# Kernel tuning notes

Hardware: AMD Instinct MI355X
Metric: run time of the kernel (lower is better)

The kernel has to match this reference:

```python
import jax, jax.numpy as jnp
import numpy as np

D_MODEL = 256
D_STATE = 16
D_CONV = 3
D_INNER = 256          # expand=1
D_HALF = D_INNER // 2  # 128
DT_RANK = 16           # ceil(256/16)
B, L0, L1 = 4, 4096, 4096


def setup_inputs() -> dict:
    key = jax.random.key(0)
    ks = jax.random.split(key, 10)
    u_0 = jax.random.normal(ks[0], (B, L0, D_MODEL), jnp.float32)
    u_1 = jax.random.normal(ks[1], (B, L1, D_MODEL), jnp.float32)
    in_proj_w = jax.random.normal(ks[2], (D_INNER, D_MODEL), jnp.float32) * (D_MODEL ** -0.5)
    conv_x_w = jax.random.normal(ks[3], (D_HALF, 1, D_CONV), jnp.float32) * (D_CONV ** -0.5)
    conv_z_w = jax.random.normal(ks[4], (D_HALF, 1, D_CONV), jnp.float32) * (D_CONV ** -0.5)
    x_proj_w = jax.random.normal(ks[5], (DT_RANK + 2 * D_STATE, D_HALF), jnp.float32) * (D_HALF ** -0.5)
    dt_init_std = DT_RANK ** -0.5
    dt_proj_w = jax.random.uniform(ks[6], (D_HALF, DT_RANK), jnp.float32, -dt_init_std, dt_init_std)
    # dt bias = inverse-softplus of dt ~ LogUniform(1e-3, 1e-1)
    dt = jnp.exp(jax.random.uniform(ks[7], (D_HALF,), jnp.float32) * (np.log(0.1) - np.log(0.001)) + np.log(0.001))
    dt = jnp.clip(dt, 1e-4, None)
    dt_proj_b = dt + jnp.log(-jnp.expm1(-dt))
    A_log = jnp.log(jnp.broadcast_to(jnp.arange(1, D_STATE + 1, dtype=jnp.float32), (D_HALF, D_STATE)))
    D_param = jnp.ones((D_HALF,), jnp.float32)
    out_proj_w = jax.random.normal(ks[8], (D_MODEL, D_INNER), jnp.float32) * (D_INNER ** -0.5)
    return {"u_0": u_0, "u_1": u_1, "in_proj_w": in_proj_w, "conv_x_w": conv_x_w,
            "conv_z_w": conv_z_w, "x_proj_w": x_proj_w, "dt_proj_w": dt_proj_w,
            "dt_proj_b": dt_proj_b, "A_log": A_log, "D": D_param, "out_proj_w": out_proj_w}


def _dwconv(x, w):
    # x: [B, C, L], w: [C, 1, K] depthwise, padding='same', no bias (conv_bias//2 == 0)
    return jax.lax.conv_general_dilated(
        x, w, window_strides=(1,), padding='SAME',
        feature_group_count=x.shape[1], dimension_numbers=('NCH', 'OIH', 'NCH'))


def _selective_scan(u, delta, A, Bm, Cm, Dv):
    # u, delta: [B, L, d]; A: [d, n]; Bm, Cm: [B, L, n]; Dv: [d]
    dA = jnp.exp(delta[..., None] * A)                       # [B, L, d, n]
    dBu = (delta * u)[..., None] * Bm[:, :, None, :]         # [B, L, d, n]
    def combine(c1, c2):
        a1, b1 = c1
        a2, b2 = c2
        return a2 * a1, a2 * b1 + b2
    _, h = jax.lax.associative_scan(combine, (dA, dBu), axis=1)  # h: [B, L, d, n]
    return jnp.einsum('bldn,bln->bld', h, Cm) + u * Dv


def _stream(u, in_proj_w, conv_x_w, conv_z_w, x_proj_w, dt_proj_w, dt_proj_b, A, D, out_proj_w):
    xz = jnp.einsum('bld,ed->ble', u, in_proj_w)             # [B, L, d_inner]
    x, z = jnp.split(xz, 2, axis=-1)                         # [B, L, d_half] each
    x = jnp.swapaxes(x, 1, 2)                                # [B, d_half, L]
    z = jnp.swapaxes(z, 1, 2)
    x_f = jax.nn.silu(_dwconv(x, conv_x_w))
    z_f = jax.nn.silu(_dwconv(z, conv_z_w))
    xf = jnp.swapaxes(x_f, 1, 2)                             # [B, L, d_half]
    dbl = jnp.einsum('bld,ed->ble', xf, x_proj_w)            # [B, L, dt_rank + 2n]
    dt, Bm, Cm = jnp.split(dbl, [DT_RANK, DT_RANK + D_STATE], axis=-1)
    dt = jnp.einsum('blr,dr->bld', dt, dt_proj_w)
    delta = jax.nn.softplus(dt + dt_proj_b)                  # delta_bias + delta_softplus
    y = _selective_scan(xf, delta, A, Bm, Cm, D)             # [B, L, d_half]
    cat = jnp.concatenate([y, jnp.swapaxes(z_f, 1, 2)], axis=-1)  # [B, L, d_inner]
    return jnp.einsum('ble,oe->blo', cat, out_proj_w)


def reference(u_0, u_1, in_proj_w, conv_x_w, conv_z_w, x_proj_w, dt_proj_w, dt_proj_b, A_log, D, out_proj_w):
    A = -jnp.exp(A_log)
    out0 = _stream(u_0, in_proj_w, conv_x_w, conv_z_w, x_proj_w, dt_proj_w, dt_proj_b, A, D, out_proj_w)
    out1 = _stream(u_1, in_proj_w, conv_x_w, conv_z_w, x_proj_w, dt_proj_w, dt_proj_b, A, D, out_proj_w)
    return (out0, out1)
```

## Files before the change

### kernel.cpp

```cpp
#include <hip/hip_runtime.h>
#include <hip/hip_bf16.h>
#include <cstdint>

#define DEV __device__ __forceinline__

typedef __attribute__((ext_vector_type(8))) short short8;
typedef __attribute__((ext_vector_type(4))) float f32x4;
typedef __attribute__((ext_vector_type(4))) unsigned short us4;
typedef __attribute__((ext_vector_type(8))) unsigned short us8;

DEV unsigned short f2bf(float x) {
    unsigned int u = __float_as_uint(x);
    unsigned int r = (u + 0x7FFFu + ((u >> 16) & 1u)) >> 16;
    return (unsigned short)r;
}
DEV float bf2f(unsigned short h) { return __uint_as_float(((unsigned int)h) << 16); }

#define LL 4096
#define DM 256
#define DH 128
#define NS 16
#define SB_TOT 8
#define CH1 32
#define NCH 128
#define LOG2E 1.44269504088896f

__global__ __launch_bounds__(256) void prep_w(
    const float* __restrict__ xpw, const float* __restrict__ dtw,
    unsigned short* __restrict__ Wb)
{
    int gid = blockIdx.x * 256 + threadIdx.x;
    if (gid >= 5120) return;
    int n = gid >> 5, k0 = (gid & 31) * 4;
    if (n < 128) {
        float a0 = 0.f, a1 = 0.f, a2 = 0.f, a3 = 0.f;
        const float* dw = dtw + n * 16;
        #pragma unroll
        for (int r = 0; r < 16; ++r) {
            float w = dw[r];
            const float* xr = xpw + r * 128 + k0;
            a0 = fmaf(w, xr[0], a0);
            a1 = fmaf(w, xr[1], a1);
            a2 = fmaf(w, xr[2], a2);
            a3 = fmaf(w, xr[3], a3);
        }
        us4 rr = { f2bf(a0), f2bf(a1), f2bf(a2), f2bf(a3) };
        *(us4*)&Wb[n * 128 + k0] = rr;
    } else {
        f32x4 v = *(const f32x4*)&xpw[(n - 112) * 128 + k0];
        us4 rr = { f2bf(v.x), f2bf(v.y), f2bf(v.z), f2bf(v.w) };
        *(us4*)&Wb[n * 128 + k0] = rr;
    }
}

template<int AF32, int F32OUT>
__global__ __launch_bounds__(256) void gemm_full(
    const float* __restrict__ Af0, const float* __restrict__ Af1,
    const unsigned short* __restrict__ Ab,
    const float* __restrict__ Bw,
    float* __restrict__ Cf, unsigned short* __restrict__ Cb)
{
    __shared__ __align__(16) unsigned short As[128 * 40];
    __shared__ __align__(16) unsigned short Bs[256 * 40];
    const int t = threadIdx.x;
    const int m0 = blockIdx.x * 128;
    const int lane = t & 63, wv = t >> 6;
    const int wm = (wv & 1) * 64, wn = (wv >> 1) * 128;
    const int lr = lane & 15, lk = (lane >> 4) * 8;
    const float* Afp = nullptr;
    if (AF32) Afp = (blockIdx.x < 128) ? (Af0 + (size_t)m0 * 256)
                                       : (Af1 + ((size_t)m0 - 16384) * 256);
    f32x4 acc[4][8] = {};
    for (int kt = 0; kt < 8; ++kt) {
        const int k0 = kt * 32;
        #pragma unroll
        for (int i = 0; i < 6; ++i) {
            int s = t + i * 256;
            int row = s >> 2, col = (s & 3) * 8;
            if (row < 128) {
                if (AF32) {
                    const float* src = Afp + (size_t)row * 256 + k0 + col;
                    f32x4 v0 = *(const f32x4*)src;
                    f32x4 v1 = *(const f32x4*)(src + 4);
                    us8 r = { f2bf(v0.x), f2bf(v0.y), f2bf(v0.z), f2bf(v0.w),
                              f2bf(v1.x), f2bf(v1.y), f2bf(v1.z), f2bf(v1.w) };
                    *(us8*)&As[row * 40 + col] = r;
                } else {
                    *(short8*)&As[row * 40 + col] =
                        *(const short8*)(Ab + (size_t)(m0 + row) * 256 + k0 + col);
                }
            } else {
                int br = row - 128;
                const float* src = Bw + (size_t)br * 256 + k0 + col;
                f32x4 v0 = *(const f32x4*)src;
                f32x4 v1 = *(const f32x4*)(src + 4);
                us8 r = { f2bf(v0.x), f2bf(v0.y), f2bf(v0.z), f2bf(v0.w),
                          f2bf(v1.x), f2bf(v1.y), f2bf(v1.z), f2bf(v1.w) };
                *(us8*)&Bs[br * 40 + col] = r;
            }
        }
        __syncthreads();
        short8 av[4];
        #pragma unroll
        for (int i = 0; i < 4; ++i) av[i] = *(const short8*)&As[(wm + i * 16 + lr) * 40 + lk];
        #pragma unroll
        for (int j = 0; j < 8; ++j) {
            short8 bv = *(const short8*)&Bs[(wn + j * 16 + lr) * 40 + lk];
            #pragma unroll
            for (int i = 0; i < 4; ++i)
                acc[i][j] = __builtin_amdgcn_mfma_f32_16x16x32_bf16(av[i], bv, acc[i][j], 0, 0, 0);
        }
        __syncthreads();
    }
    #pragma unroll
    for (int i = 0; i < 4; ++i) {
        #pragma unroll
        for (int j = 0; j < 8; ++j) {
            int r0 = m0 + wm + i * 16 + (lane >> 4) * 4;
            int cc = wn + j * 16 + lr;
            #pragma unroll
            for (int r = 0; r < 4; ++r) {
                float v = acc[i][j][r];
                if (F32OUT) Cf[(size_t)(r0 + r) * 256 + cc] = v;
                else        Cb[(size_t)(r0 + r) * 256 + cc] = f2bf(v);
            }
        }
    }
}

__global__ __launch_bounds__(256) void convproj(
    const unsigned short* __restrict__ xz, const unsigned short* __restrict__ Wb,
    const float* __restrict__ wx, const float* __restrict__ wz,
    const float* __restrict__ dtb,
    float* __restrict__ xf, unsigned short* __restrict__ catb,
    float* __restrict__ delta, float* __restrict__ BC)
{
    __shared__ __align__(16) unsigned short Bs[160 * 136];
    __shared__ __align__(16) unsigned short As[64 * 136];
    const int t = threadIdx.x;
    const int m0 = blockIdx.x * 64;
    for (int q = t; q < 2560; q += 256) {
        int n = q >> 4, kc = (q & 15) * 8;
        *(short8*)&Bs[n * 136 + kc] = *(const short8*)(Wb + n * 128 + kc);
    }
    #pragma unroll
    for (int i = 0; i < 8; ++i) {
        int s = t + i * 256;
        int r = s >> 5, g = s & 31;
        int gr = m0 + r;
        int l = gr & 4095;
        int c; const float* wp; const unsigned short* bp;
        if (g < 16) { c = g * 8;        wp = wx; bp = xz + (size_t)gr * 256 + c; }
        else        { c = (g - 16) * 8; wp = wz; bp = xz + (size_t)gr * 256 + 128 + c; }
        us8 zz = (us8)0;
        us8 vm = (l > 0)    ? *(const us8*)(bp - 256) : zz;
        us8 v0 = *(const us8*)bp;
        us8 vp = (l < 4095) ? *(const us8*)(bp + 256) : zz;
        float o[8];
        #pragma unroll
        for (int j = 0; j < 8; ++j) {
            int cc = c + j;
            float v = bf2f(vm[j]) * wp[cc * 3] + bf2f(v0[j]) * wp[cc * 3 + 1]
                    + bf2f(vp[j]) * wp[cc * 3 + 2];
            v = v / (1.f + __expf(-v));
            o[j] = v;
        }
        us8 rb = { f2bf(o[0]), f2bf(o[1]), f2bf(o[2]), f2bf(o[3]),
                   f2bf(o[4]), f2bf(o[5]), f2bf(o[6]), f2bf(o[7]) };
        if (g < 16) {
            *(us8*)&As[r * 136 + c] = rb;
            *(f32x4*)&xf[(size_t)gr * 128 + c]     = *(f32x4*)&o[0];
            *(f32x4*)&xf[(size_t)gr * 128 + c + 4] = *(f32x4*)&o[4];
        } else {
            *(us8*)&catb[(size_t)gr * 256 + 128 + c] = rb;
        }
    }
    __syncthreads();
    const int lane = t & 63, wv = t >> 6;
    const int lr = lane & 15, lk = (lane >> 4) * 8;
    f32x4 acc[10] = {};
    #pragma unroll
    for (int kt = 0; kt < 4; ++kt) {
        const int k0 = kt * 32;
        short8 av = *(const short8*)&As[(wv * 16 + lr) * 136 + k0 + lk];
        #pragma unroll
        for (int j = 0; j < 10; ++j) {
            short8 bv = *(const short8*)&Bs[(j * 16 + lr) * 136 + k0 + lk];
            acc[j] = __builtin_amdgcn_mfma_f32_16x16x32_bf16(av, bv, acc[j], 0, 0, 0);
        }
    }
    const int r0 = (lane >> 4) * 4;
    #pragma unroll
    for (int j = 0; j < 10; ++j) {
        int col = j * 16 + lr;
        #pragma unroll
        for (int r = 0; r < 4; ++r) {
            float v = acc[j][r];
            size_t row = (size_t)m0 + wv * 16 + r0 + r;
            if (j < 8) {
                float x = v + dtb[col];
                float sp = (x > 20.f) ? x : log1pf(__expf(x));
                delta[row * 128 + col] = sp;
            } else {
                BC[row * 32 + (col - 128)] = v;
            }
        }
    }
}

__global__ __launch_bounds__(128) void scan_p1(
    const float* __restrict__ delta, const float* __restrict__ xf,
    const float* __restrict__ BC, const float* __restrict__ alog,
    float* __restrict__ P, float* __restrict__ H)
{
    __shared__ float dt_s[CH1 * 128];
    __shared__ float du_s[CH1 * 128];
    __shared__ float b_s[CH1 * 16];
    int t = threadIdx.x;
    int ch = blockIdx.x, sb = blockIdx.y;
    size_t rb = (size_t)sb * LL + (size_t)ch * CH1;
    for (int q = t; q < CH1 * 32; q += 128) {
        int row = q >> 5, c4 = (q & 31) * 4;
        f32x4 dv = *(const f32x4*)&delta[(rb + row) * DH + c4];
        f32x4 uv = *(const f32x4*)&xf[(rb + row) * DH + c4];
        *(f32x4*)&dt_s[row * 128 + c4] = dv;
        f32x4 duv = dv * uv;
        *(f32x4*)&du_s[row * 128 + c4] = duv;
    }
    {
        int q = t & 127;
        int row = q >> 2, c4 = (q & 3) * 4;
        *(f32x4*)&b_s[row * 16 + c4] = *(const f32x4*)&BC[(rb + row) * 32 + c4];
    }
    __syncthreads();
    float Ar[16];
    #pragma unroll
    for (int n = 0; n < 16; ++n) Ar[n] = -__expf(alog[t * 16 + n]) * LOG2E;
    float h[16], p[16];
    #pragma unroll
    for (int n = 0; n < 16; ++n) { h[n] = 0.f; p[n] = 1.f; }
    for (int i = 0; i < CH1; ++i) {
        float dt = dt_s[i * 128 + t];
        float du = du_s[i * 128 + t];
        float bl[16];
        *(f32x4*)&bl[0]  = *(const f32x4*)&b_s[i * 16];
        *(f32x4*)&bl[4]  = *(const f32x4*)&b_s[i * 16 + 4];
        *(f32x4*)&bl[8]  = *(const f32x4*)&b_s[i * 16 + 8];
        *(f32x4*)&bl[12] = *(const f32x4*)&b_s[i * 16 + 12];
        #pragma unroll
        for (int n = 0; n < 16; ++n) {
            float a = exp2f(dt * Ar[n]);
            h[n] = fmaf(a, h[n], du * bl[n]);
            p[n] *= a;
        }
    }
    size_t ob = (((size_t)sb * NCH + ch) * 128 + t) * 16;
    #pragma unroll
    for (int n4 = 0; n4 < 16; n4 += 4) {
        f32x4 pv = { p[n4], p[n4 + 1], p[n4 + 2], p[n4 + 3] };
        f32x4 hv = { h[n4], h[n4 + 1], h[n4 + 2], h[n4 + 3] };
        *(f32x4*)&P[ob + n4] = pv;
        *(f32x4*)&H[ob + n4] = hv;
    }
}

__global__ __launch_bounds__(256) void scan_p2(const float* __restrict__ P, float* __restrict__ H)
{
    __shared__ float Ps[NCH * 16], Hs[NCH * 16];
    int t = threadIdx.x;
    int d = blockIdx.x, sb = blockIdx.y;
    for (int q = t; q < NCH * 4; q += 256) {
        int ch = q >> 2, c4 = (q & 3) * 4;
        size_t g = (((size_t)sb * NCH + ch) * 128 + d) * 16 + c4;
        *(f32x4*)&Ps[ch * 16 + c4] = *(const f32x4*)&P[g];
        *(f32x4*)&Hs[ch * 16 + c4] = *(const f32x4*)&H[g];
    }
    __syncthreads();
    if (t < 16) {
        float hin = 0.f;
        for (int c = 0; c < NCH; ++c) {
            float pp = Ps[c * 16 + t], hl = Hs[c * 16 + t];
            Hs[c * 16 + t] = hin;
            hin = fmaf(pp, hin, hl);
        }
    }
    __syncthreads();
    for (int q = t; q < NCH * 4; q += 256) {
        int ch = q >> 2, c4 = (q & 3) * 4;
        size_t g = (((size_t)sb * NCH + ch) * 128 + d) * 16 + c4;
        *(f32x4*)&H[g] = *(const f32x4*)&Hs[ch * 16 + c4];
    }
}

__global__ __launch_bounds__(128) void scan_p3(
    const float* __restrict__ delta, const float* __restrict__ xf,
    const float* __restrict__ BC, const float* __restrict__ alog,
    const float* __restrict__ Dp, const float* __restrict__ H,
    unsigned short* __restrict__ catb)
{
    __shared__ float dt_s[CH1 * 128];
    __shared__ float u_s[CH1 * 128];
    __shared__ float b_s[CH1 * 16];
    __shared__ float c_s[CH1 * 16];
    int t = threadIdx.x;
    int ch = blockIdx.x, sb = blockIdx.y;
    size_t rb = (size_t)sb * LL + (size_t)ch * CH1;
    for (int q = t; q < CH1 * 32; q += 128) {
        int row = q >> 5, c4 = (q & 31) * 4;
        *(f32x4*)&dt_s[row * 128 + c4] = *(const f32x4*)&delta[(rb + row) * DH + c4];
        *(f32x4*)&u_s[row * 128 + c4]  = *(const f32x4*)&xf[(rb + row) * DH + c4];
    }
    {
        int q = t & 127;
        int row = q >> 2, c4 = (q & 3) * 4;
        *(f32x4*)&b_s[row * 16 + c4] = *(const f32x4*)&BC[(rb + row) * 32 + c4];
        *(f32x4*)&c_s[row * 16 + c4] = *(const f32x4*)&BC[(rb + row) * 32 + 16 + c4];
    }
    __syncthreads();
    float Ar[16];
    #pragma unroll
    for (int n = 0; n < 16; ++n) Ar[n] = -__expf(alog[t * 16 + n]) * LOG2E;
    float Dv = Dp[t];
    size_t ob = (((size_t)sb * NCH + ch) * 128 + t) * 16;
    float h[16];
    #pragma unroll
    for (int n4 = 0; n4 < 16; n4 += 4) {
        f32x4 hv = *(const f32x4*)&H[ob + n4];
        h[n4] = hv.x; h[n4 + 1] = hv.y; h[n4 + 2] = hv.z; h[n4 + 3] = hv.w;
    }
    for (int i = 0; i < CH1; ++i) {
        float dt = dt_s[i * 128 + t];
        float uu = u_s[i * 128 + t];
        float du = dt * uu;
        float bl[16], cl[16];
        *(f32x4*)&bl[0]  = *(const f32x4*)&b_s[i * 16];
        *(f32x4*)&bl[4]  = *(const f32x4*)&b_s[i * 16 + 4];
        *(f32x4*)&bl[8]  = *(const f32x4*)&b_s[i * 16 + 8];
        *(f32x4*)&bl[12] = *(const f32x4*)&b_s[i * 16 + 12];
        *(f32x4*)&cl[0]  = *(const f32x4*)&c_s[i * 16];
        *(f32x4*)&cl[4]  = *(const f32x4*)&c_s[i * 16 + 4];
        *(f32x4*)&cl[8]  = *(const f32x4*)&c_s[i * 16 + 8];
        *(f32x4*)&cl[12] = *(const f32x4*)&c_s[i * 16 + 12];
        float y0 = uu * Dv, y1 = 0.f, y2 = 0.f, y3 = 0.f;
        #pragma unroll
        for (int n = 0; n < 16; n += 4) {
            float a0 = exp2f(dt * Ar[n]);
            float a1 = exp2f(dt * Ar[n + 1]);
            float a2 = exp2f(dt * Ar[n + 2]);
            float a3 = exp2f(dt * Ar[n + 3]);
            h[n]     = fmaf(a0, h[n],     du * bl[n]);
            h[n + 1] = fmaf(a1, h[n + 1], du * bl[n + 1]);
            h[n + 2] = fmaf(a2, h[n + 2], du * bl[n + 2]);
            h[n + 3] = fmaf(a3, h[n + 3], du * bl[n + 3]);
            y0 = fmaf(h[n],     cl[n],     y0);
            y1 = fmaf(h[n + 1], cl[n + 1], y1);
            y2 = fmaf(h[n + 2], cl[n + 2], y2);
            y3 = fmaf(h[n + 3], cl[n + 3], y3);
        }
        float y = (y0 + y1) + (y2 + y3);
        catb[(rb + i) * DM + t] = f2bf(y);
    }
}

extern "C" void kernel_launch(void* const* d_in, const int* in_sizes, int n_in,
                              void* d_out, int out_size, void* d_ws, size_t ws_size,
                              hipStream_t stream) {
    const float* u0   = (const float*)d_in[0];
    const float* u1   = (const float*)d_in[1];
    const float* inw  = (const float*)d_in[2];
    const float* cxw  = (const float*)d_in[3];
    const float* czw  = (const float*)d_in[4];
    const float* xpw  = (const float*)d_in[5];
    const float* dtw  = (const float*)d_in[6];
    const float* dtb  = (const float*)d_in[7];
    const float* alog = (const float*)d_in[8];
    const float* Dp   = (const float*)d_in[9];
    const float* outw = (const float*)d_in[10];

    char* ws = (char*)d_ws;
    unsigned short* xzbf = (unsigned short*)(ws + 0);
    float* P             = (float*)(ws + 0);
    float* H             = (float*)(ws + 8388608);
    float* delta         = (float*)(ws + 16777216);
    float* xf            = (float*)(ws + 33554432);
    float* BC            = (float*)(ws + 50331648);
    unsigned short* catb = (unsigned short*)(ws + 54525952);
    unsigned short* Wb   = (unsigned short*)(ws + 71303168);

    float* outp = (float*)d_out;

    prep_w<<<20, 256, 0, stream>>>(xpw, dtw, Wb);
    gemm_full<1, 0><<<256, 256, 0, stream>>>(u0, u1, nullptr, inw, nullptr, xzbf);
    convproj<<<512, 256, 0, stream>>>(xzbf, Wb, cxw, czw, dtb, xf, catb, delta, BC);
    scan_p1<<<dim3(NCH, 8), 128, 0, stream>>>(delta, xf, BC, alog, P, H);
    scan_p2<<<dim3(128, 8), 256, 0, stream>>>(P, H);
    scan_p3<<<dim3(NCH, 8), 128, 0, stream>>>(delta, xf, BC, alog, Dp, H, catb);
    gemm_full<0, 1><<<256, 256, 0, stream>>>(nullptr, nullptr, catb, outw, outp, nullptr);
}
```

Measured before the change: 237.1 us.

## Pre-convert inputs and weights to bf16 and use direct-to-LDS loads in GEMMs

Adds a prep kernel that converts both input streams and the in/out projection weights to bf16 once, alongside the existing x_proj/dt weight folding. Both GEMMs become a single bf16 B-transposed kernel with 128x128 tiles on a 2D grid. The kernel fills shared memory with global_load_lds and no longer converts fp32 per tile. This removes the per-block weight conversion, and the smaller tiles mean more blocks. In exchange it adds a full extra read/write pass over the activations, and the unpadded LDS rows may cause bank conflicts. Workspace buffers are reshuffled so the new bf16 input buffer aliases delta.

Result: faster. 224.7 us (-5.2%).

```diff
diff --git a/kernel.cpp b/kernel.cpp
--- a/kernel.cpp
+++ b/kernel.cpp
@@ -15,6 +15,12 @@
     return (unsigned short)r;
 }
 DEV float bf2f(unsigned short h) { return __uint_as_float(((unsigned int)h) << 16); }
+
+DEV void gld_lds16(const unsigned short* g, unsigned short* l) {
+    __builtin_amdgcn_global_load_lds(
+        (const __attribute__((address_space(1))) unsigned int*)g,
+        (__attribute__((address_space(3))) unsigned int*)l, 16, 0, 0);
+}
 
 #define LL 4096
 #define DM 256
@@ -25,99 +31,103 @@
 #define NCH 128
 #define LOG2E 1.44269504088896f
 
-__global__ __launch_bounds__(256) void prep_w(
+__global__ __launch_bounds__(256) void prep_kernel(
+    const float* __restrict__ u0, const float* __restrict__ u1,
+    const float* __restrict__ inw, const float* __restrict__ outw,
     const float* __restrict__ xpw, const float* __restrict__ dtw,
-    unsigned short* __restrict__ Wb)
+    unsigned short* __restrict__ ubf, unsigned short* __restrict__ wbi,
+    unsigned short* __restrict__ wbo, unsigned short* __restrict__ Wb)
 {
     int gid = blockIdx.x * 256 + threadIdx.x;
-    if (gid >= 5120) return;
-    int n = gid >> 5, k0 = (gid & 31) * 4;
-    if (n < 128) {
-        float a0 = 0.f, a1 = 0.f, a2 = 0.f, a3 = 0.f;
-        const float* dw = dtw + n * 16;
-        #pragma unroll
-        for (int r = 0; r < 16; ++r) {
-            float w = dw[r];
-            const float* xr = xpw + r * 128 + k0;
-            a0 = fmaf(w, xr[0], a0);
-            a1 = fmaf(w, xr[1], a1);
-            a2 = fmaf(w, xr[2], a2);
-            a3 = fmaf(w, xr[3], a3);
-        }
-        us4 rr = { f2bf(a0), f2bf(a1), f2bf(a2), f2bf(a3) };
-        *(us4*)&Wb[n * 128 + k0] = rr;
-    } else {
-        f32x4 v = *(const f32x4*)&xpw[(n - 112) * 128 + k0];
-        us4 rr = { f2bf(v.x), f2bf(v.y), f2bf(v.z), f2bf(v.w) };
-        *(us4*)&Wb[n * 128 + k0] = rr;
-    }
-}
-
-template<int AF32, int F32OUT>
-__global__ __launch_bounds__(256) void gemm_full(
-    const float* __restrict__ Af0, const float* __restrict__ Af1,
-    const unsigned short* __restrict__ Ab,
-    const float* __restrict__ Bw,
+    int i = gid * 4;
+    if (i < 4194304) {
+        f32x4 v = *(const f32x4*)&u0[i];
+        us4 r = { f2bf(v.x), f2bf(v.y), f2bf(v.z), f2bf(v.w) };
+        *(us4*)&ubf[i] = r;
+    } else if (i < 8388608) {
+        int j = i - 4194304;
+        f32x4 v = *(const f32x4*)&u1[j];
+        us4 r = { f2bf(v.x), f2bf(v.y), f2bf(v.z), f2bf(v.w) };
+        *(us4*)&ubf[4194304 + j] = r;
+    } else if (i < 8454144) {
+        int j = i - 8388608;
+        f32x4 v = *(const f32x4*)&inw[j];
+        us4 r = { f2bf(v.x), f2bf(v.y), f2bf(v.z), f2bf(v.w) };
+        *(us4*)&wbi[j] = r;
+    } else if (i < 8519680) {
+        int j = i - 8454144;
+        f32x4 v = *(const f32x4*)&outw[j];
+        us4 r = { f2bf(v.x), f2bf(v.y), f2bf(v.z), f2bf(v.w) };
+        *(us4*)&wbo[j] = r;
+    } else if (i < 8540160) {
+        int j = i - 8519680;
+        int n = j >> 7, k0 = j & 127;
+        if (n < 128) {
+            float a0 = 0.f, a1 = 0.f, a2 = 0.f, a3 = 0.f;
+            const float* dw = dtw + n * 16;
+            #pragma unroll
+            for (int r = 0; r < 16; ++r) {
+                float w = dw[r];
+                const float* xr = xpw + r * 128 + k0;
+                a0 = fmaf(w, xr[0], a0);
+                a1 = fmaf(w, xr[1], a1);
+                a2 = fmaf(w, xr[2], a2);
+                a3 = fmaf(w, xr[3], a3);
+            }
+            us4 rr = { f2bf(a0), f2bf(a1), f2bf(a2), f2bf(a3) };
+            *(us4*)&Wb[n * 128 + k0] = rr;
+        } else {
+            f32x4 v = *(const f32x4*)&xpw[(n - 112) * 128 + k0];
+            us4 rr = { f2bf(v.x), f2bf(v.y), f2bf(v.z), f2bf(v.w) };
+            *(us4*)&Wb[n * 128 + k0] = rr;
+        }
+    }
+}
+
+template<int F32OUT>
+__global__ __launch_bounds__(256) void gemm_bt(
+    const unsigned short* __restrict__ A, const unsigned short* __restrict__ B,
     float* __restrict__ Cf, unsigned short* __restrict__ Cb)
 {
-    __shared__ __align__(16) unsigned short As[128 * 40];
-    __shared__ __align__(16) unsigned short Bs[256 * 40];
+    __shared__ __align__(16) unsigned short As[128 * 32];
+    __shared__ __align__(16) unsigned short Bs[128 * 32];
     const int t = threadIdx.x;
-    const int m0 = blockIdx.x * 128;
+    const int m0 = blockIdx.x * 128, n0 = blockIdx.y * 128;
     const int lane = t & 63, wv = t >> 6;
-    const int wm = (wv & 1) * 64, wn = (wv >> 1) * 128;
+    const int wm = (wv & 1) * 64, wn = (wv >> 1) * 64;
     const int lr = lane & 15, lk = (lane >> 4) * 8;
-    const float* Afp = nullptr;
-    if (AF32) Afp = (blockIdx.x < 128) ? (Af0 + (size_t)m0 * 256)
-                                       : (Af1 + ((size_t)m0 - 16384) * 256);
-    f32x4 acc[4][8] = {};
+    const int srow = lane >> 2, scol = (lane & 3) * 8;
+
+    f32x4 acc[4][4] = {};
     for (int kt = 0; kt < 8; ++kt) {
         const int k0 = kt * 32;
         #pragma unroll
-        for (int i = 0; i < 6; ++i) {
-            int s = t + i * 256;
-            int row = s >> 2, col = (s & 3) * 8;
-            if (row < 128) {
-                if (AF32) {
-                    const float* src = Afp + (size_t)row * 256 + k0 + col;
-                    f32x4 v0 = *(const f32x4*)src;
-                    f32x4 v1 = *(const f32x4*)(src + 4);
-                    us8 r = { f2bf(v0.x), f2bf(v0.y), f2bf(v0.z), f2bf(v0.w),
-                              f2bf(v1.x), f2bf(v1.y), f2bf(v1.z), f2bf(v1.w) };
-                    *(us8*)&As[row * 40 + col] = r;
-                } else {
-                    *(short8*)&As[row * 40 + col] =
-                        *(const short8*)(Ab + (size_t)(m0 + row) * 256 + k0 + col);
-                }
-            } else {
-                int br = row - 128;
-                const float* src = Bw + (size_t)br * 256 + k0 + col;
-                f32x4 v0 = *(const f32x4*)src;
-                f32x4 v1 = *(const f32x4*)(src + 4);
-                us8 r = { f2bf(v0.x), f2bf(v0.y), f2bf(v0.z), f2bf(v0.w),
-                          f2bf(v1.x), f2bf(v1.y), f2bf(v1.z), f2bf(v1.w) };
-                *(us8*)&Bs[br * 40 + col] = r;
-            }
+        for (int h = 0; h < 2; ++h) {
+            const int c = wv + h * 4;
+            const unsigned short* ga = A + (size_t)(m0 + c * 16 + srow) * 256 + k0 + scol;
+            const unsigned short* gb = B + (size_t)(n0 + c * 16 + srow) * 256 + k0 + scol;
+            gld_lds16(ga, &As[c * 512]);
+            gld_lds16(gb, &Bs[c * 512]);
         }
         __syncthreads();
-        short8 av[4];
-        #pragma unroll
-        for (int i = 0; i < 4; ++i) av[i] = *(const short8*)&As[(wm + i * 16 + lr) * 40 + lk];
-        #pragma unroll
-        for (int j = 0; j < 8; ++j) {
-            short8 bv = *(const short8*)&Bs[(wn + j * 16 + lr) * 40 + lk];
+        short8 av[4], bv[4];
+        #pragma unroll
+        for (int i = 0; i < 4; ++i) av[i] = *(const short8*)&As[(wm + i * 16 + lr) * 32 + lk];
+        #pragma unroll
+        for (int i = 0; i < 4; ++i) bv[i] = *(const short8*)&Bs[(wn + i * 16 + lr) * 32 + lk];
+        #pragma unroll
+        for (int i = 0; i < 4; ++i)
             #pragma unroll
-            for (int i = 0; i < 4; ++i)
-                acc[i][j] = __builtin_amdgcn_mfma_f32_16x16x32_bf16(av[i], bv, acc[i][j], 0, 0, 0);
-        }
+            for (int j = 0; j < 4; ++j)
+                acc[i][j] = __builtin_amdgcn_mfma_f32_16x16x32_bf16(av[i], bv[j], acc[i][j], 0, 0, 0);
         __syncthreads();
     }
     #pragma unroll
     for (int i = 0; i < 4; ++i) {
         #pragma unroll
-        for (int j = 0; j < 8; ++j) {
+        for (int j = 0; j < 4; ++j) {
             int r0 = m0 + wm + i * 16 + (lane >> 4) * 4;
-            int cc = wn + j * 16 + lr;
+            int cc = n0 + wn + j * 16 + lr;
             #pragma unroll
             for (int r = 0; r < 4; ++r) {
                 float v = acc[i][j][r];
@@ -378,22 +388,25 @@
     const float* outw = (const float*)d_in[10];
 
     char* ws = (char*)d_ws;
-    unsigned short* xzbf = (unsigned short*)(ws + 0);
-    float* P             = (float*)(ws + 0);
-    float* H             = (float*)(ws + 8388608);
-    float* delta         = (float*)(ws + 16777216);
+    unsigned short* ubf  = (unsigned short*)(ws + 0);
+    float* delta         = (float*)(ws + 0);
+    unsigned short* xzbf = (unsigned short*)(ws + 16777216);
+    float* P             = (float*)(ws + 16777216);
+    float* H             = (float*)(ws + 25165824);
     float* xf            = (float*)(ws + 33554432);
     float* BC            = (float*)(ws + 50331648);
     unsigned short* catb = (unsigned short*)(ws + 54525952);
-    unsigned short* Wb   = (unsigned short*)(ws + 71303168);
+    unsigned short* wbi  = (unsigned short*)(ws + 71303168);
+    unsigned short* wbo  = (unsigned short*)(ws + 71434240);
+    unsigned short* Wb   = (unsigned short*)(ws + 71565312);
 
     float* outp = (float*)d_out;
 
-    prep_w<<<20, 256, 0, stream>>>(xpw, dtw, Wb);
-    gemm_full<1, 0><<<256, 256, 0, stream>>>(u0, u1, nullptr, inw, nullptr, xzbf);
+    prep_kernel<<<8340, 256, 0, stream>>>(u0, u1, inw, outw, xpw, dtw, ubf, wbi, wbo, Wb);
+    gemm_bt<0><<<dim3(256, 2), 256, 0, stream>>>(ubf, wbi, nullptr, xzbf);
     convproj<<<512, 256, 0, stream>>>(xzbf, Wb, cxw, czw, dtb, xf, catb, delta, BC);
     scan_p1<<<dim3(NCH, 8), 128, 0, stream>>>(delta, xf, BC, alog, P, H);
     scan_p2<<<dim3(128, 8), 256, 0, stream>>>(P, H);
     scan_p3<<<dim3(NCH, 8), 128, 0, stream>>>(delta, xf, BC, alog, Dp, H, catb);
-    gemm_full<0, 1><<<256, 256, 0, stream>>>(nullptr, nullptr, catb, outw, outp, nullptr);
-}
+    gemm_bt<1><<<dim3(256, 2), 256, 0, stream>>>(catb, wbo, outp, nullptr);
+}
```
